# Optimization experiments

Hardware: AMD Instinct MI355X
Metric: run time of the kernel (lower is better)

The kernel has to match this reference:

```python
import jax, jax.numpy as jnp
import numpy as np

G = 64        # supervoxel grid per dim (cfg.orig_grid_shape)
CELL = 16     # pixels per grid cell
T = 32        # tile size in px (covers 2x2 cells)
NT = 32       # tiles per dim per shift config
CH = 40       # Conv_trio channels


def setup_inputs() -> dict:
    key = jax.random.key(0)
    ks = jax.random.split(key, 8)
    W = G * CELL
    curr_image = jax.random.normal(ks[0], (W, W), jnp.float32)
    # masks encode per-pixel supervoxel id (pixel belongs to cell floor(px/CELL))
    ids = (jnp.arange(G)[:, None] * G + jnp.arange(G)[None, :]).astype(jnp.float32)
    masks = jnp.repeat(jnp.repeat(ids, CELL, axis=0), CELL, axis=1)[..., None]
    return {
        'curr_image': curr_image,
        'masks': masks,
        'conv1_w': jax.random.normal(ks[1], (3, 3, 1, CH), jnp.float32) * 0.1,
        'conv1_b': jnp.zeros((CH,), jnp.float32),
        'ln1_s': jnp.ones((CH,), jnp.float32),
        'ln1_b': jnp.zeros((CH,), jnp.float32),
        'conv2_w': jax.random.normal(ks[2], (3, 3, CH, CH), jnp.float32) * 0.1,
        'conv2_b': jnp.zeros((CH,), jnp.float32),
        'ln2_s': jnp.ones((CH,), jnp.float32),
        'ln2_b': jnp.zeros((CH,), jnp.float32),
        'dense_w': jax.random.normal(ks[3], ((T // 4) * (T // 4) * CH, 6), jnp.float32) * 0.02,
        'dense_b': jnp.zeros((6,), jnp.float32),
    }


def _tile(a):
    # [W, W, c] -> [NT*NT, T, T, c]
    c = a.shape[-1]
    return a.reshape(NT, T, NT, T, c).transpose(0, 2, 1, 3, 4).reshape(NT * NT, T, T, c)


def _config_tokens(img, masks, ids, sx, sy):
    # shifted tiling: tile (i,j) covers px [T*i + sx*CELL, ...)
    rolled_img = jnp.roll(img, (-sx * CELL, -sy * CELL), (0, 1))
    rolled_msk = jnp.roll(masks, (-sx * CELL, -sy * CELL), (0, 1))
    img_t = _tile(rolled_img)          # [NT*NT, T, T, 1]
    msk_t = _tile(rolled_msk)[..., 0]  # [NT*NT, T, T]
    curr_ids = ids[sx::2, sy::2].reshape(-1)  # [NT*NT]
    filt = (msk_t == curr_ids[:, None, None]).astype(img_t.dtype)
    return img_t * filt[..., None]


def _conv_trio(x, w, b, s, bln):
    y = jax.lax.conv_general_dilated(x, w, (2, 2), 'SAME',
                                     dimension_numbers=('NHWC', 'HWIO', 'NHWC')) + b
    mu = jnp.mean(y, axis=-1, keepdims=True)
    var = jnp.var(y, axis=-1, keepdims=True)
    y = (y - mu) * jax.lax.rsqrt(var + 1e-6) * s + bln
    return jax.nn.gelu(y)


def reference(curr_image, masks, conv1_w, conv1_b, ln1_s, ln1_b,
              conv2_w, conv2_b, ln2_s, ln2_b, dense_w, dense_b):
    img = curr_image[..., None]  # [W, W, 1]
    ids = (jnp.arange(G)[:, None] * G + jnp.arange(G)[None, :]).astype(masks.dtype)
    tokens = jnp.concatenate([
        _config_tokens(img, masks, ids, 0, 0),
        _config_tokens(img, masks, ids, 1, 0),
        _config_tokens(img, masks, ids, 0, 1),
        _config_tokens(img, masks, ids, 1, 1),
    ], axis=0)  # [4*NT*NT, T, T, 1]
    x = _conv_trio(tokens, conv1_w, conv1_b, ln1_s, ln1_b)  # [F, 16, 16, 40]
    x = _conv_trio(x, conv2_w, conv2_b, ln2_s, ln2_b)       # [F, 8, 8, 40]
    x = x.reshape(x.shape[0], -1)
    return x @ dense_w + dense_b  # node embeddings [F, 6]
```

## Files before the change

### kernel.cpp

```cpp
#include <hip/hip_runtime.h>
#include <math.h>

#define CH 40
#define IMW 1024
#define TOKH (9*10*40)
#define W2T_HALVES (48*48*8)
#define Z1_OFF W2T_HALVES
#define OUTC_OFF (Z1_OFF + 40)

typedef _Float16 v8h __attribute__((ext_vector_type(8)));
typedef float    v4f __attribute__((ext_vector_type(4)));
typedef float    v2f __attribute__((ext_vector_type(2)));

__device__ __forceinline__ float gelu_fast(float x) {
    float u = 1.5957691216057308f * (x + 0.044715f * x * x * x);
    return x * __builtin_amdgcn_rcpf(1.0f + __expf(-u));
}

__global__ __launch_bounds__(256) void prep_kernel(
    const float* __restrict__ w2,
    const float* __restrict__ b1, const float* __restrict__ s1,
    const float* __restrict__ bb1,
    const float* __restrict__ b2, const float* __restrict__ s2,
    const float* __restrict__ bb2,
    const float* __restrict__ dw, const float* __restrict__ db,
    _Float16* __restrict__ ws)
{
    const int t = threadIdx.x;
    int idx0 = blockIdx.x * 256 + t;
    for (int idx = idx0; idx < W2T_HALVES; idx += gridDim.x * 256) {
        int j   = idx & 7;
        int co  = (idx >> 3) % 48;
        int kgg = idx / (48 * 8);
        int k   = kgg * 8 + j;
        float v = 0.0f;
        if (co < CH && k < 360) {
            int wi = k / 40, ci = k - wi * 40;
            v = w2[(wi * CH + ci) * CH + co];
        }
        ws[idx] = (_Float16)v;
    }
    if (blockIdx.x != 0) return;

    __shared__ float zs[40];
    __shared__ float w2sum[9][40];
    __shared__ float p2l[120];
    __shared__ float red[4][6];

    if (t < 120) p2l[t] = (t < 40) ? b2[t] : (t < 80 ? s2[t - 40] : bb2[t - 80]);

    if (t >= 64 && t < 128) {
        int lane = t - 64;
        bool act = lane < CH;
        float bv = act ? b1[lane] : 0.f;
        float s = bv;
        #pragma unroll
        for (int m = 1; m < 64; m <<= 1) s += __shfl_xor(s, m, 64);
        float mu = s * (1.0f / CH);
        float d = act ? (bv - mu) : 0.f;
        float q = d * d;
        #pragma unroll
        for (int m = 1; m < 64; m <<= 1) q += __shfl_xor(q, m, 64);
        float rs = rsqrtf(q * (1.0f / CH) + 1e-6f);
        if (act) {
            float g = gelu_fast((bv - mu) * rs * s1[lane] + bb1[lane]);
            zs[lane] = g;
            ws[Z1_OFF + lane] = (_Float16)g;
        }
    }
    __syncthreads();

    for (int idx = t; idx < 360; idx += 256) {
        int wi = idx / 40, ch = idx - wi * 40;
        float s = 0.f;
        #pragma unroll
        for (int ci = 0; ci < CH; ci++)
            s += w2[(wi * CH + ci) * CH + ch] * zs[ci];
        w2sum[wi][ch] = s;
    }
    __syncthreads();

    {
        const int m = t >> 2, sub = t & 3;
        const int p = m >> 3, q = m & 7;
        const int co0 = sub * 10;
        float a6[6] = {0.f, 0.f, 0.f, 0.f, 0.f, 0.f};
        if (p >= 4 || q >= 4) {
            const int drmax = (p == 7) ? 2 : 3;
            const int dcmax = (q == 7) ? 2 : 3;
            float vv[10];
            float s_own = 0.f;
            #pragma unroll
            for (int u = 0; u < 10; u++) {
                float v = p2l[co0 + u];
                for (int dr = 0; dr < drmax; dr++)
                    for (int dc = 0; dc < dcmax; dc++)
                        v += w2sum[dr * 3 + dc][co0 + u];
                vv[u] = v; s_own += v;
            }
            s_own += __shfl_xor(s_own, 1, 64);
            s_own += __shfl_xor(s_own, 2, 64);
            float mu = s_own * (1.0f / CH);
            float v_own = 0.f;
            #pragma unroll
            for (int u = 0; u < 10; u++) { float d = vv[u] - mu; v_own += d * d; }
            v_own += __shfl_xor(v_own, 1, 64);
            v_own += __shfl_xor(v_own, 2, 64);
            float rs = rsqrtf(v_own * (1.0f / CH) + 1e-6f);
            const float* wp = &dw[(m * CH + co0) * 6];
            #pragma unroll
            for (int u = 0; u < 10; u++) {
                float gv = gelu_fast((vv[u] - mu) * rs * p2l[40 + co0 + u] + p2l[80 + co0 + u]);
                v2f w01 = *(const v2f*)&wp[u * 6];
                v2f w23 = *(const v2f*)&wp[u * 6 + 2];
                v2f w45 = *(const v2f*)&wp[u * 6 + 4];
                a6[0] += gv * w01[0]; a6[1] += gv * w01[1];
                a6[2] += gv * w23[0]; a6[3] += gv * w23[1];
                a6[4] += gv * w45[0]; a6[5] += gv * w45[1];
            }
        }
        #pragma unroll
        for (int off = 32; off > 0; off >>= 1)
            #pragma unroll
            for (int k = 0; k < 6; k++) a6[k] += __shfl_down(a6[k], off, 64);
        int wv = t >> 6, lane = t & 63;
        if (lane == 0) {
            #pragma unroll
            for (int k = 0; k < 6; k++) red[wv][k] = a6[k];
        }
        __syncthreads();
        if (t == 0) {
            float* oc = (float*)&ws[OUTC_OFF];
            #pragma unroll
            for (int k = 0; k < 6; k++)
                oc[k] = red[0][k] + red[1][k] + red[2][k] + red[3][k] + db[k];
        }
    }
}

__global__ __launch_bounds__(256) void sgn_kernel(
    const float* __restrict__ img,
    const float* __restrict__ w1, const float* __restrict__ b1,
    const float* __restrict__ s1, const float* __restrict__ bb1,
    const float* __restrict__ b2, const float* __restrict__ s2,
    const float* __restrict__ bb2,
    const float* __restrict__ dw,
    const _Float16* __restrict__ ws,
    float* __restrict__ out)
{
    __shared__ __align__(16) _Float16 x1h[4 * TOKH];
    __shared__ float w1t[40 * 12];
    __shared__ float p1s[120];
    __shared__ float p2s[120];
    __shared__ unsigned koff_s[48];

    const int t    = threadIdx.x;
    const int wv   = t >> 6;
    const int lane = t & 63;

    for (int i = t; i < 360; i += 256) {
        int k = i / 40, ch = i - k * 40;
        w1t[ch * 12 + k] = w1[i];
    }
    if (t < 120) {
        p1s[t] = (t < 40) ? b1[t] : (t < 80 ? s1[t - 40] : bb1[t - 80]);
    } else if (t >= 128 && t < 248) {
        int i = t - 128;
        p2s[i] = (i < 40) ? b2[i] : (i < 80 ? s2[i - 40] : bb2[i - 80]);
    }
    if (t < 48) {
        int k0 = 8 * t;
        unsigned v = 0;
        if (k0 < 360) {
            int wi = k0 / 40, ci0 = k0 - wi * 40;
            int dr = wi / 3, dc = wi - 3 * dr;
            v = (unsigned)((dr * 10 + dc) * 40 + ci0);
        }
        koff_s[t] = v;
    }
    __syncthreads();

    const int f   = blockIdx.x * 4 + wv;
    const int cfg = f >> 10;
    const int ij  = f & 1023;
    const int ti  = ij >> 5, tj = ij & 31;
    const int cr  = 2 * ti + (cfg & 1);
    const int cc  = 2 * tj + (cfg >> 1);
    _Float16* x1w = &x1h[wv * TOKH];

    {
        const int r = lane >> 3, c = lane & 7;
        const float* ib = &img[(cr * 16) * IMW + cc * 16];
        float vin[9];
        #pragma unroll
        for (int dr = 0; dr < 3; dr++)
            #pragma unroll
            for (int dc = 0; dc < 3; dc++) {
                int rr = 2 * r + dr, cp = 2 * c + dc;
                vin[dr * 3 + dc] = (rr < 16 && cp < 16) ? ib[rr * IMW + cp] : 0.0f;
            }
        float y[40];
        float s = 0.f;
        #pragma unroll
        for (int ch = 0; ch < 40; ch++) {
            float a = p1s[ch];
            const float* wr = &w1t[ch * 12];
            #pragma unroll
            for (int k = 0; k < 9; k++) a += vin[k] * wr[k];
            y[ch] = a; s += a;
        }
        float mu = s * (1.0f / CH);
        float q = 0.f;
        #pragma unroll
        for (int ch = 0; ch < 40; ch++) { float d = y[ch] - mu; q += d * d; }
        float rs = rsqrtf(q * (1.0f / CH) + 1e-6f);
        const int base = (r * 10 + c) * 40;
        #pragma unroll
        for (int chk = 0; chk < 5; chk++) {
            v8h hv;
            #pragma unroll
            for (int jj = 0; jj < 8; jj++) {
                int ch = chk * 8 + jj;
                hv[jj] = (_Float16)gelu_fast((y[ch] - mu) * rs * p1s[40 + ch] + p1s[80 + ch]);
            }
            *(v8h*)&x1w[base + chk * 8] = hv;
        }
    }
    if (lane < 17) {
        int rr = (lane < 9) ? 8 : (lane - 9);
        int cb = (lane < 9) ? lane : 8;
        const v8h* zsrc = (const v8h*)&ws[Z1_OFF];
        int base = (rr * 10 + cb) * 40;
        *(v8h*)&x1w[base]      = zsrc[0];
        *(v8h*)&x1w[base + 8]  = zsrc[1];
        *(v8h*)&x1w[base + 16] = zsrc[2];
        *(v8h*)&x1w[base + 24] = zsrc[3];
        *(v8h*)&x1w[base + 32] = zsrc[4];
    }
    __builtin_amdgcn_s_waitcnt(0);

    v4f acc0 = {0,0,0,0}, acc1 = {0,0,0,0}, acc2 = {0,0,0,0};
    const int row = lane & 15;
    const int kg  = lane >> 4;
    {
        const unsigned pbase = (unsigned)((20 * (row >> 2) + 2 * (row & 3)) * 40);
        #pragma unroll
        for (int s = 0; s < 12; s++) {
            const int kc = (s << 2) | kg;
            unsigned aoff = pbase + koff_s[kc];
            v8h a = *(const v8h*)&x1w[aoff];
            const _Float16* wb = &ws[(kc * 48 + row) * 8];
            v8h bf0 = *(const v8h*)&wb[0];
            v8h bf1 = *(const v8h*)&wb[16 * 8];
            v8h bf2 = *(const v8h*)&wb[32 * 8];
            acc0 = __builtin_amdgcn_mfma_f32_16x16x32_f16(a, bf0, acc0, 0, 0, 0);
            acc1 = __builtin_amdgcn_mfma_f32_16x16x32_f16(a, bf1, acc1, 0, 0, 0);
            acc2 = __builtin_amdgcn_mfma_f32_16x16x32_f16(a, bf2, acc2, 0, 0, 0);
        }
    }

    {
        const int cix = row;
        const bool h2 = (cix < 8);
        const float b2a = p2s[cix],      b2b = p2s[16 + cix],  b2c = h2 ? p2s[32 + cix] : 0.f;
        const float s2a = p2s[40 + cix], s2b = p2s[56 + cix],  s2c = h2 ? p2s[72 + cix] : 0.f;
        const float g2a = p2s[80 + cix], g2b = p2s[96 + cix],  g2c = h2 ? p2s[112 + cix] : 0.f;
        float a6[6] = {0.f, 0.f, 0.f, 0.f, 0.f, 0.f};
        #pragma unroll
        for (int j = 0; j < 4; j++) {
            const int m = (kg << 2) | j;
            float v0 = acc0[j] + b2a;
            float v1 = acc1[j] + b2b;
            float v2 = h2 ? (acc2[j] + b2c) : 0.f;
            float s = v0 + v1 + v2;
            s += __shfl_xor(s, 1, 64);
            s += __shfl_xor(s, 2, 64);
            s += __shfl_xor(s, 4, 64);
            s += __shfl_xor(s, 8, 64);
            float mu = s * (1.0f / CH);
            float d0 = v0 - mu, d1 = v1 - mu, d2 = v2 - mu;
            float q = d0 * d0 + d1 * d1 + (h2 ? d2 * d2 : 0.f);
            q += __shfl_xor(q, 1, 64);
            q += __shfl_xor(q, 2, 64);
            q += __shfl_xor(q, 4, 64);
            q += __shfl_xor(q, 8, 64);
            float rs = rsqrtf(q * (1.0f / CH) + 1e-6f);
            float g0 = gelu_fast(d0 * rs * s2a + g2a);
            float g1 = gelu_fast(d1 * rs * s2b + g2b);
            float g2 = h2 ? gelu_fast(d2 * rs * s2c + g2c) : 0.f;
            const int drow = ((m >> 2) * 8 + (m & 3)) * CH;
            const float* w0p = &dw[(drow + cix) * 6];
            const float* w1p = &dw[(drow + 16 + cix) * 6];
            const float* w2p = &dw[(drow + 32 + cix) * 6];
            #pragma unroll
            for (int k = 0; k < 6; k++)
                a6[k] += g0 * w0p[k] + g1 * w1p[k] + g2 * w2p[k];
        }
        #pragma unroll
        for (int off = 32; off > 0; off >>= 1)
            #pragma unroll
            for (int k = 0; k < 6; k++) a6[k] += __shfl_down(a6[k], off, 64);
        if (lane == 0) {
            const float* oc = (const float*)&ws[OUTC_OFF];
            #pragma unroll
            for (int k = 0; k < 6; k++) out[f * 6 + k] = a6[k] + oc[k];
        }
    }
}

extern "C" void kernel_launch(void* const* d_in, const int* in_sizes, int n_in,
                              void* d_out, int out_size, void* d_ws, size_t ws_size,
                              hipStream_t stream) {
    const float* img = (const float*)d_in[0];
    const float* w1  = (const float*)d_in[2];
    const float* b1  = (const float*)d_in[3];
    const float* s1  = (const float*)d_in[4];
    const float* bb1 = (const float*)d_in[5];
    const float* w2  = (const float*)d_in[6];
    const float* b2  = (const float*)d_in[7];
    const float* s2  = (const float*)d_in[8];
    const float* bb2 = (const float*)d_in[9];
    const float* dw  = (const float*)d_in[10];
    const float* db  = (const float*)d_in[11];
    float* out = (float*)d_out;
    _Float16* ws = (_Float16*)d_ws;

    prep_kernel<<<32, 256, 0, stream>>>(w2, b1, s1, bb1, b2, s2, bb2, dw, db, ws);
    sgn_kernel<<<1024, 256, 0, stream>>>(img, w1, b1, s1, bb1,
                                         b2, s2, bb2, dw, ws, out);
}
```

Measured before the change: 32.59 us.

## Fuse weight-prep kernel into main kernel, recomputing per block in LDS

Drops the separate prep kernel. Each block now builds the fp16 transposed conv2 weights in shared memory, computes the padding-constant z1, and computes the constant output term for masked-out positions itself. This removes one kernel launch and the dependency between the two kernels. In exchange, every one of 1024 blocks redoes the weight transposition (about 15K halves), the w2sum reduction and the constant-output computation, and uses more LDS per block, which may lower occupancy.

```diff
diff --git a/kernel.cpp b/kernel.cpp
--- a/kernel.cpp
+++ b/kernel.cpp
@@ -4,9 +4,7 @@
 #define CH 40
 #define IMW 1024
 #define TOKH (9*10*40)
-#define W2T_HALVES (48*48*8)
-#define Z1_OFF W2T_HALVES
-#define OUTC_OFF (Z1_OFF + 40)
+#define W2TN (48*40*8)
 
 typedef _Float16 v8h __attribute__((ext_vector_type(8)));
 typedef float    v4f __attribute__((ext_vector_type(4)));
@@ -17,40 +15,79 @@
     return x * __builtin_amdgcn_rcpf(1.0f + __expf(-u));
 }
 
-__global__ __launch_bounds__(256) void prep_kernel(
-    const float* __restrict__ w2,
-    const float* __restrict__ b1, const float* __restrict__ s1,
-    const float* __restrict__ bb1,
-    const float* __restrict__ b2, const float* __restrict__ s2,
-    const float* __restrict__ bb2,
+__global__ __launch_bounds__(256) void sgn_kernel(
+    const float* __restrict__ img,
+    const float* __restrict__ w1, const float* __restrict__ b1,
+    const float* __restrict__ s1, const float* __restrict__ bb1,
+    const float* __restrict__ w2, const float* __restrict__ b2,
+    const float* __restrict__ s2, const float* __restrict__ bb2,
     const float* __restrict__ dw, const float* __restrict__ db,
-    _Float16* __restrict__ ws)
+    float* __restrict__ out)
 {
-    const int t = threadIdx.x;
-    int idx0 = blockIdx.x * 256 + t;
-    for (int idx = idx0; idx < W2T_HALVES; idx += gridDim.x * 256) {
-        int j   = idx & 7;
-        int co  = (idx >> 3) % 48;
-        int kgg = idx / (48 * 8);
-        int k   = kgg * 8 + j;
-        float v = 0.0f;
-        if (co < CH && k < 360) {
-            int wi = k / 40, ci = k - wi * 40;
-            v = w2[(wi * CH + ci) * CH + co];
-        }
-        ws[idx] = (_Float16)v;
-    }
-    if (blockIdx.x != 0) return;
-
+    __shared__ __align__(16) _Float16 w2t[W2TN + 64];
+    __shared__ __align__(16) _Float16 x1h[4 * TOKH];
+    __shared__ float w1t[40 * 12];
+    __shared__ float p1s[120];
+    __shared__ float p2s[120];
     __shared__ float zs[40];
     __shared__ float w2sum[9][40];
-    __shared__ float p2l[120];
+    __shared__ unsigned koff_s[48];
     __shared__ float red[4][6];
-
-    if (t < 120) p2l[t] = (t < 40) ? b2[t] : (t < 80 ? s2[t - 40] : bb2[t - 80]);
-
-    if (t >= 64 && t < 128) {
-        int lane = t - 64;
+    __shared__ float outc[6];
+
+    const int t    = threadIdx.x;
+    const int wv   = t >> 6;
+    const int lane = t & 63;
+
+    const int f   = blockIdx.x * 4 + wv;
+    const int cfg = f >> 10;
+    const int ij  = f & 1023;
+    const int ti  = ij >> 5, tj = ij & 31;
+    const int cr  = 2 * ti + (cfg & 1);
+    const int cc  = 2 * tj + (cfg >> 1);
+
+    float vin[9];
+    {
+        const int r = lane >> 3, c = lane & 7;
+        const float* ib = &img[(cr * 16) * IMW + cc * 16];
+        #pragma unroll
+        for (int dr = 0; dr < 3; dr++)
+            #pragma unroll
+            for (int dc = 0; dc < 3; dc++) {
+                int rr = 2 * r + dr, cp = 2 * c + dc;
+                vin[dr * 3 + dc] = (rr < 16 && cp < 16) ? ib[rr * IMW + cp] : 0.0f;
+            }
+    }
+
+    for (int i = t; i < W2TN; i += 256) {
+        int j  = i & 7;
+        int co = (i >> 3) % 40;
+        int kc = i / 320;
+        int k  = kc * 8 + j;
+        float v = (k < 360) ? w2[k * 40 + co] : 0.0f;
+        w2t[i] = (_Float16)v;
+    }
+    for (int i = t; i < 360; i += 256) {
+        int k = i / 40, ch = i - k * 40;
+        w1t[ch * 12 + k] = w1[i];
+    }
+    if (t < 120) {
+        p1s[t] = (t < 40) ? b1[t] : (t < 80 ? s1[t - 40] : bb1[t - 80]);
+    } else if (t >= 128 && t < 248) {
+        int i = t - 128;
+        p2s[i] = (i < 40) ? b2[i] : (i < 80 ? s2[i - 40] : bb2[i - 80]);
+    }
+    if (t < 48) {
+        int k0 = 8 * t;
+        unsigned v = 0;
+        if (k0 < 360) {
+            int wi = k0 / 40, ci0 = k0 - wi * 40;
+            int dr = wi / 3, dc = wi - 3 * dr;
+            v = (unsigned)((dr * 10 + dc) * 40 + ci0);
+        }
+        koff_s[t] = v;
+    }
+    if (wv == 0) {
         bool act = lane < CH;
         float bv = act ? b1[lane] : 0.f;
         float s = bv;
@@ -62,21 +99,60 @@
         #pragma unroll
         for (int m = 1; m < 64; m <<= 1) q += __shfl_xor(q, m, 64);
         float rs = rsqrtf(q * (1.0f / CH) + 1e-6f);
-        if (act) {
-            float g = gelu_fast((bv - mu) * rs * s1[lane] + bb1[lane]);
-            zs[lane] = g;
-            ws[Z1_OFF + lane] = (_Float16)g;
-        }
+        if (act) zs[lane] = gelu_fast((bv - mu) * rs * s1[lane] + bb1[lane]);
     }
     __syncthreads();
 
-    for (int idx = t; idx < 360; idx += 256) {
-        int wi = idx / 40, ch = idx - wi * 40;
+    for (int i = t; i < 360; i += 256) {
+        int wi = i / 40, ch = i - wi * 40;
         float s = 0.f;
         #pragma unroll
         for (int ci = 0; ci < CH; ci++)
             s += w2[(wi * CH + ci) * CH + ch] * zs[ci];
         w2sum[wi][ch] = s;
+    }
+    _Float16* x1w = &x1h[wv * TOKH];
+    {
+        const int r = lane >> 3, c = lane & 7;
+        float y[40];
+        float s = 0.f;
+        #pragma unroll
+        for (int ch = 0; ch < 40; ch++) {
+            float a = p1s[ch];
+            const float* wr = &w1t[ch * 12];
+            #pragma unroll
+            for (int k = 0; k < 9; k++) a += vin[k] * wr[k];
+            y[ch] = a; s += a;
+        }
+        float mu = s * (1.0f / CH);
+        float q = 0.f;
+        #pragma unroll
+        for (int ch = 0; ch < 40; ch++) { float d = y[ch] - mu; q += d * d; }
+        float rs = rsqrtf(q * (1.0f / CH) + 1e-6f);
+        const int base = (r * 10 + c) * 40;
+        #pragma unroll
+        for (int chk = 0; chk < 5; chk++) {
+            v8h hv;
+            #pragma unroll
+            for (int jj = 0; jj < 8; jj++) {
+                int ch = chk * 8 + jj;
+                hv[jj] = (_Float16)gelu_fast((y[ch] - mu) * rs * p1s[40 + ch] + p1s[80 + ch]);
+            }
+            *(v8h*)&x1w[base + chk * 8] = hv;
+        }
+    }
+    if (lane < 17) {
+        int rr = (lane < 9) ? 8 : (lane - 9);
+        int cb = (lane < 9) ? lane : 8;
+        int base = (rr * 10 + cb) * 40;
+        #pragma unroll
+        for (int chk = 0; chk < 5; chk++) {
+            v8h hv;
+            #pragma unroll
+            for (int jj = 0; jj < 8; jj++)
+                hv[jj] = (_Float16)zs[chk * 8 + jj];
+            *(v8h*)&x1w[base + chk * 8] = hv;
+        }
     }
     __syncthreads();
 
@@ -92,7 +168,7 @@
             float s_own = 0.f;
             #pragma unroll
             for (int u = 0; u < 10; u++) {
-                float v = p2l[co0 + u];
+                float v = p2s[co0 + u];
                 for (int dr = 0; dr < drmax; dr++)
                     for (int dc = 0; dc < dcmax; dc++)
                         v += w2sum[dr * 3 + dc][co0 + u];
@@ -110,7 +186,7 @@
             const float* wp = &dw[(m * CH + co0) * 6];
             #pragma unroll
             for (int u = 0; u < 10; u++) {
-                float gv = gelu_fast((vv[u] - mu) * rs * p2l[40 + co0 + u] + p2l[80 + co0 + u]);
+                float gv = gelu_fast((vv[u] - mu) * rs * p2s[40 + co0 + u] + p2s[80 + co0 + u]);
                 v2f w01 = *(const v2f*)&wp[u * 6];
                 v2f w23 = *(const v2f*)&wp[u * 6 + 2];
                 v2f w45 = *(const v2f*)&wp[u * 6 + 4];
@@ -123,121 +199,18 @@
         for (int off = 32; off > 0; off >>= 1)
             #pragma unroll
             for (int k = 0; k < 6; k++) a6[k] += __shfl_down(a6[k], off, 64);
-        int wv = t >> 6, lane = t & 63;
         if (lane == 0) {
             #pragma unroll
             for (int k = 0; k < 6; k++) red[wv][k] = a6[k];
         }
-        __syncthreads();
-        if (t == 0) {
-            float* oc = (float*)&ws[OUTC_OFF];
-            #pragma unroll
-            for (int k = 0; k < 6; k++)
-                oc[k] = red[0][k] + red[1][k] + red[2][k] + red[3][k] + db[k];
-        }
-    }
-}
-
-__global__ __launch_bounds__(256) void sgn_kernel(
-    const float* __restrict__ img,
-    const float* __restrict__ w1, const float* __restrict__ b1,
-    const float* __restrict__ s1, const float* __restrict__ bb1,
-    const float* __restrict__ b2, const float* __restrict__ s2,
-    const float* __restrict__ bb2,
-    const float* __restrict__ dw,
-    const _Float16* __restrict__ ws,
-    float* __restrict__ out)
-{
-    __shared__ __align__(16) _Float16 x1h[4 * TOKH];
-    __shared__ float w1t[40 * 12];
-    __shared__ float p1s[120];
-    __shared__ float p2s[120];
-    __shared__ unsigned koff_s[48];
-
-    const int t    = threadIdx.x;
-    const int wv   = t >> 6;
-    const int lane = t & 63;
-
-    for (int i = t; i < 360; i += 256) {
-        int k = i / 40, ch = i - k * 40;
-        w1t[ch * 12 + k] = w1[i];
-    }
-    if (t < 120) {
-        p1s[t] = (t < 40) ? b1[t] : (t < 80 ? s1[t - 40] : bb1[t - 80]);
-    } else if (t >= 128 && t < 248) {
-        int i = t - 128;
-        p2s[i] = (i < 40) ? b2[i] : (i < 80 ? s2[i - 40] : bb2[i - 80]);
-    }
-    if (t < 48) {
-        int k0 = 8 * t;
-        unsigned v = 0;
-        if (k0 < 360) {
-            int wi = k0 / 40, ci0 = k0 - wi * 40;
-            int dr = wi / 3, dc = wi - 3 * dr;
-            v = (unsigned)((dr * 10 + dc) * 40 + ci0);
-        }
-        koff_s[t] = v;
     }
     __syncthreads();
-
-    const int f   = blockIdx.x * 4 + wv;
-    const int cfg = f >> 10;
-    const int ij  = f & 1023;
-    const int ti  = ij >> 5, tj = ij & 31;
-    const int cr  = 2 * ti + (cfg & 1);
-    const int cc  = 2 * tj + (cfg >> 1);
-    _Float16* x1w = &x1h[wv * TOKH];
-
-    {
-        const int r = lane >> 3, c = lane & 7;
-        const float* ib = &img[(cr * 16) * IMW + cc * 16];
-        float vin[9];
-        #pragma unroll
-        for (int dr = 0; dr < 3; dr++)
-            #pragma unroll
-            for (int dc = 0; dc < 3; dc++) {
-                int rr = 2 * r + dr, cp = 2 * c + dc;
-                vin[dr * 3 + dc] = (rr < 16 && cp < 16) ? ib[rr * IMW + cp] : 0.0f;
-            }
-        float y[40];
-        float s = 0.f;
-        #pragma unroll
-        for (int ch = 0; ch < 40; ch++) {
-            float a = p1s[ch];
-            const float* wr = &w1t[ch * 12];
-            #pragma unroll
-            for (int k = 0; k < 9; k++) a += vin[k] * wr[k];
-            y[ch] = a; s += a;
-        }
-        float mu = s * (1.0f / CH);
-        float q = 0.f;
-        #pragma unroll
-        for (int ch = 0; ch < 40; ch++) { float d = y[ch] - mu; q += d * d; }
-        float rs = rsqrtf(q * (1.0f / CH) + 1e-6f);
-        const int base = (r * 10 + c) * 40;
-        #pragma unroll
-        for (int chk = 0; chk < 5; chk++) {
-            v8h hv;
-            #pragma unroll
-            for (int jj = 0; jj < 8; jj++) {
-                int ch = chk * 8 + jj;
-                hv[jj] = (_Float16)gelu_fast((y[ch] - mu) * rs * p1s[40 + ch] + p1s[80 + ch]);
-            }
-            *(v8h*)&x1w[base + chk * 8] = hv;
-        }
-    }
-    if (lane < 17) {
-        int rr = (lane < 9) ? 8 : (lane - 9);
-        int cb = (lane < 9) ? lane : 8;
-        const v8h* zsrc = (const v8h*)&ws[Z1_OFF];
-        int base = (rr * 10 + cb) * 40;
-        *(v8h*)&x1w[base]      = zsrc[0];
-        *(v8h*)&x1w[base + 8]  = zsrc[1];
-        *(v8h*)&x1w[base + 16] = zsrc[2];
-        *(v8h*)&x1w[base + 24] = zsrc[3];
-        *(v8h*)&x1w[base + 32] = zsrc[4];
-    }
-    __builtin_amdgcn_s_waitcnt(0);
+    if (t == 0) {
+        #pragma unroll
+        for (int k = 0; k < 6; k++)
+            outc[k] = red[0][k] + red[1][k] + red[2][k] + red[3][k] + db[k];
+    }
+    __syncthreads();
 
     v4f acc0 = {0,0,0,0}, acc1 = {0,0,0,0}, acc2 = {0,0,0,0};
     const int row = lane & 15;
@@ -249,7 +222,7 @@
             const int kc = (s << 2) | kg;
             unsigned aoff = pbase + koff_s[kc];
             v8h a = *(const v8h*)&x1w[aoff];
-            const _Float16* wb = &ws[(kc * 48 + row) * 8];
+            const _Float16* wb = &w2t[(kc * 40 + row) * 8];
             v8h bf0 = *(const v8h*)&wb[0];
             v8h bf1 = *(const v8h*)&wb[16 * 8];
             v8h bf2 = *(const v8h*)&wb[32 * 8];
@@ -258,7 +231,6 @@
             acc2 = __builtin_amdgcn_mfma_f32_16x16x32_f16(a, bf2, acc2, 0, 0, 0);
         }
     }
-
     {
         const int cix = row;
         const bool h2 = (cix < 8);
@@ -301,9 +273,8 @@
             #pragma unroll
             for (int k = 0; k < 6; k++) a6[k] += __shfl_down(a6[k], off, 64);
         if (lane == 0) {
-            const float* oc = (const float*)&ws[OUTC_OFF];
-            #pragma unroll
-            for (int k = 0; k < 6; k++) out[f * 6 + k] = a6[k] + oc[k];
+            #pragma unroll
+            for (int k = 0; k < 6; k++) out[f * 6 + k] = a6[k] + outc[k];
         }
     }
 }
@@ -323,9 +294,7 @@
     const float* dw  = (const float*)d_in[10];
     const float* db  = (const float*)d_in[11];
     float* out = (float*)d_out;
-    _Float16* ws = (_Float16*)d_ws;
-
-    prep_kernel<<<32, 256, 0, stream>>>(w2, b1, s1, bb1, b2, s2, bb2, dw, db, ws);
+
     sgn_kernel<<<1024, 256, 0, stream>>>(img, w1, b1, s1, bb1,
-                                         b2, s2, bb2, dw, ws, out);
+                                         w2, b2, s2, bb2, dw, db, out);
 }
```

Result: slower. 62.34 us (+91.3%).
